# Optimization experiments

Measured on AMD Instinct MI355X. Metric: run time of the kernel, lower is better.

Reference implementation:

```python
import jax, jax.numpy as jnp
import numpy as np
import math

B, S, D, H, L = 2, 1024, 512, 8, 6
DK = D // H
DFF, V, MAXSEQ = 2048, 32000, 1024
EPS = 1e-6

def make_pe(max_len, d):
    pos = np.arange(max_len)[:, None].astype(np.float32)
    div = np.exp(np.arange(0, d, 2).astype(np.float32) * -(math.log(10000.0) / d))
    pe = np.zeros((max_len, d), np.float32)
    pe[:, 0::2] = np.sin(pos * div)
    pe[:, 1::2] = np.cos(pos * div)
    return jnp.asarray(pe)

PE = make_pe(5000, D)  # fixed sinusoidal buffer (non-learned)

def layer_norm(x, a, b):
    mean = jnp.mean(x, axis=-1, keepdims=True)
    std = jnp.std(x, axis=-1, ddof=1, keepdims=True)  # torch .std is unbiased
    return a * (x - mean) / (std + EPS) + b

def linear(x, W, b):
    # torch nn.Linear: y = x @ W.T + b, W is [out, in]
    return jnp.einsum('...i,oi->...o', x, W) + b

def rel_attention(q, k, v, mask4, pos_embeds):
    # q,k,v: [B,H,S,DK]; mask4: [B,1,S,S] int; pos_embeds: [H, MAXSEQ+1, DK]
    scale = 1.0 / math.sqrt(DK)
    scores = jnp.einsum('bhqd,bhkd->bhqk', q, k) * scale
    nz = (mask4 != 0).astype(jnp.int32)
    csum = (jnp.cumsum(mask4, axis=-1) - 1) * nz * S          # [B,1,S,S]
    offset = jnp.arange(S)[None, :]                            # [1,S] -> broadcasts over rows
    indices = (offset + csum) * nz                             # flat idx m*S + l into per-(b,h) [S,S]
    pe = pos_embeds[:, :S]                                     # [H,S,DK]
    rel = jnp.einsum('bhld,hmd->bhml', q, pe) * scale          # [B,H,S,S]
    idx = jnp.broadcast_to(indices, (B, H, S, S)).reshape(B, H, S * S)
    rel_g = jnp.take_along_axis(rel.reshape(B, H, S * S), idx, axis=-1)
    rel_g = rel_g.reshape(B, H, S, S) * nz.astype(scores.dtype)
    scores = jnp.where(mask4 == 0, -1e9, scores + rel_g)
    p = jax.nn.softmax(scores, axis=-1)
    return jnp.einsum('bhqk,bhkd->bhqd', p, v)

def reference(inp, inp_mask, emb, Wq, bq, Wk, bk, Wv, bv, Wo, bo, rel,
              ln1a, ln1b, ln2a, ln2b, W1, b1, W2, b2, lnfa, lnfb, Wg, bg):
    x = emb[inp] * math.sqrt(D) + PE[None, :S]   # embed + sinusoidal PE
    mask4 = inp_mask[:, None]                     # [B,1,S,S]
    for i in range(L):
        h = layer_norm(x, ln1a[i], ln1b[i])
        q = linear(h, Wq[i], bq[i]).reshape(B, S, H, DK).transpose(0, 2, 1, 3)
        k = linear(h, Wk[i], bk[i]).reshape(B, S, H, DK).transpose(0, 2, 1, 3)
        v = linear(h, Wv[i], bv[i]).reshape(B, S, H, DK).transpose(0, 2, 1, 3)
        a = rel_attention(q, k, v, mask4, rel[i])
        a = a.transpose(0, 2, 1, 3).reshape(B, S, D)
        x = x + linear(a, Wo[i], bo[i])
        h2 = layer_norm(x, ln2a[i], ln2b[i])
        x = x + linear(jax.nn.relu(linear(h2, W1[i], b1[i])), W2[i], b2[i])
    x = layer_norm(x, lnfa, lnfb)
    return jax.nn.log_softmax(linear(x, Wg, bg), axis=-1)

def setup_inputs() -> dict:
    key = jax.random.key(0)
    ks = jax.random.split(key, 16)
    rn = lambda k, shp, s=0.02: jax.random.normal(k, shp, jnp.float32) * s
    inp = jax.random.randint(ks[0], (B, S), 0, V, dtype=jnp.int32)
    inp_mask = jnp.broadcast_to(jnp.tril(jnp.ones((S, S), jnp.int32)), (B, S, S))
    return {
        'inp': inp, 'inp_mask': inp_mask,
        'emb': rn(ks[1], (V, D), 1.0),
        'Wq': rn(ks[2], (L, D, D)), 'bq': jnp.zeros((L, D), jnp.float32),
        'Wk': rn(ks[3], (L, D, D)), 'bk': jnp.zeros((L, D), jnp.float32),
        'Wv': rn(ks[4], (L, D, D)), 'bv': jnp.zeros((L, D), jnp.float32),
        'Wo': rn(ks[5], (L, D, D)), 'bo': jnp.zeros((L, D), jnp.float32),
        'rel': rn(ks[6], (L, H, MAXSEQ + 1, DK), 1.0),
        'ln1a': jnp.ones((L, D), jnp.float32), 'ln1b': jnp.zeros((L, D), jnp.float32),
        'ln2a': jnp.ones((L, D), jnp.float32), 'ln2b': jnp.zeros((L, D), jnp.float32),
        'W1': rn(ks[7], (L, DFF, D)), 'b1': jnp.zeros((L, DFF), jnp.float32),
        'W2': rn(ks[8], (L, D, DFF)), 'b2': jnp.zeros((L, D), jnp.float32),
        'lnfa': jnp.ones((D,), jnp.float32), 'lnfb': jnp.zeros((D,), jnp.float32),
        'Wg': rn(ks[9], (V, D)), 'bg': jnp.zeros((V,), jnp.float32),
    }
```

## Files before the change

kernel.cpp:

```cpp
#include <hip/hip_runtime.h>
#include <math.h>

typedef __bf16 bf16;
typedef __bf16 bf16x8 __attribute__((ext_vector_type(8)));
typedef __bf16 bf16x4 __attribute__((ext_vector_type(4)));
typedef __bf16 bf16x2 __attribute__((ext_vector_type(2)));
typedef float f32x4 __attribute__((ext_vector_type(4)));

#define B_ 2
#define S_ 1024
#define D_ 512
#define H_ 8
#define L_ 6
#define DK_ 64
#define DFF_ 2048
#define V_ 32000
#define MAXSEQ_ 1024
#define M_ 2048
#define QKV_ 1536

#define GLDS16(g, l) __builtin_amdgcn_global_load_lds((const __attribute__((address_space(1))) void*)(g), (__attribute__((address_space(3))) void*)(l), 16, 0, 0)

__device__ inline float blockReduceSum(float v, float* red) {
  for (int off = 32; off; off >>= 1) v += __shfl_xor(v, off, 64);
  int wid = threadIdx.x >> 6;
  __syncthreads();
  if ((threadIdx.x & 63) == 0) red[wid] = v;
  __syncthreads();
  return red[0] + red[1] + red[2] + red[3];
}

__global__ __launch_bounds__(256) void convw_kernel(const float* __restrict__ src,
                                                    bf16* __restrict__ dst, int n) {
  int i = (blockIdx.x * 256 + threadIdx.x) * 4;
  if (i < n) {
    float4 v = *(const float4*)(src + i);
    dst[i]     = (bf16)v.x;
    dst[i + 1] = (bf16)v.y;
    dst[i + 2] = (bf16)v.z;
    dst[i + 3] = (bf16)v.w;
  }
}

__global__ __launch_bounds__(256) void convqkv_kernel(const float* __restrict__ Wq,
                                                      const float* __restrict__ Wk,
                                                      const float* __restrict__ Wv,
                                                      bf16* __restrict__ dst) {
  int i = (blockIdx.x * 256 + threadIdx.x) * 4;
  int l = i / (QKV_ * D_);
  int rem = i - l * (QKV_ * D_);
  int r = rem >> 9;
  int c = i & (D_ - 1);
  int which = r >> 9, rr = r & 511;
  const float* src = (which == 0 ? Wq : which == 1 ? Wk : Wv) + ((size_t)l * D_ + rr) * D_ + c;
  float4 v = *(const float4*)src;
  dst[i]     = (bf16)v.x;
  dst[i + 1] = (bf16)v.y;
  dst[i + 2] = (bf16)v.z;
  dst[i + 3] = (bf16)v.w;
}

__global__ __launch_bounds__(256) void convbqkv_kernel(const float* __restrict__ bq,
                                                       const float* __restrict__ bk,
                                                       const float* __restrict__ bv,
                                                       float* __restrict__ dst) {
  int i = blockIdx.x * 256 + threadIdx.x;
  if (i >= L_ * QKV_) return;
  int l = i / QKV_, r = i - l * QKV_;
  int which = r >> 9, rr = r & 511;
  const float* s = (which == 0 ? bq : which == 1 ? bk : bv);
  dst[i] = s[l * D_ + rr];
}

__global__ __launch_bounds__(256) void embed_kernel(const int* __restrict__ inp,
                                                    const float* __restrict__ emb,
                                                    float* __restrict__ x) {
  int i = blockIdx.x * 256 + threadIdx.x;
  int d = i & (D_ - 1);
  int s = (i >> 9) & (S_ - 1);
  int b = i >> 19;
  int tok = inp[b * S_ + s];
  int j2 = d & ~1;
  float div = expf(-(float)j2 * (9.210340371976184f / (float)D_));
  float ang = (float)s * div;
  float pe = (d & 1) ? cosf(ang) : sinf(ang);
  x[i] = emb[(size_t)tok * D_ + d] * 22.627416997969522f + pe;
}

__global__ __launch_bounds__(256) void ln_kernel(const float* __restrict__ X,
                                                 const float* __restrict__ ga,
                                                 const float* __restrict__ gb,
                                                 bf16* __restrict__ out) {
  __shared__ float red[4];
  int row = blockIdx.x;
  const float* xr = X + (size_t)row * D_;
  int t = threadIdx.x;
  float x0 = xr[t], x1 = xr[t + 256];
  float mean = blockReduceSum(x0 + x1, red) * (1.0f / (float)D_);
  float d0 = x0 - mean, d1 = x1 - mean;
  float var = blockReduceSum(d0 * d0 + d1 * d1, red) * (1.0f / (float)(D_ - 1));
  float rs = 1.0f / (sqrtf(var) + 1e-6f);
  bf16* orow = out + (size_t)row * D_;
  orow[t]       = (bf16)(ga[t] * d0 * rs + gb[t]);
  orow[t + 256] = (bf16)(ga[t + 256] * d1 * rs + gb[t + 256]);
}

template <int EPI>
__global__ __launch_bounds__(256) void gemm128(const bf16* __restrict__ A,
                                               const bf16* __restrict__ W,
                                               const float* __restrict__ bias,
                                               void* __restrict__ Yv,
                                               const float* __restrict__ res,
                                               int M, int N, int K) {
  __shared__ __align__(16) bf16 As[128 * 32];
  __shared__ __align__(16) bf16 Bs[128 * 32];
  int t = threadIdx.x;
  int lane = t & 63, w = t >> 6;
  int n0 = blockIdx.x * 128, m0 = blockIdx.y * 128;
  int sr = lane >> 2, sc = (lane & 3) * 8;
  const bf16* ag0 = A + (size_t)(m0 + w * 16 + sr) * K + sc;
  const bf16* ag1 = A + (size_t)(m0 + (w + 4) * 16 + sr) * K + sc;
  const bf16* wg0 = W + (size_t)(n0 + w * 16 + sr) * K + sc;
  const bf16* wg1 = W + (size_t)(n0 + (w + 4) * 16 + sr) * K + sc;
  bf16* la0 = &As[w * 512];
  bf16* la1 = &As[(w + 4) * 512];
  bf16* lb0 = &Bs[w * 512];
  bf16* lb1 = &Bs[(w + 4) * 512];
  int wm = (w >> 1) * 64, wn = (w & 1) * 64;
  int fr = lane & 15, fk = (lane >> 4) * 8;
  f32x4 acc[4][4] = {};
  for (int kt = 0; kt < K; kt += 32) {
    GLDS16(ag0 + kt, la0);
    GLDS16(ag1 + kt, la1);
    GLDS16(wg0 + kt, lb0);
    GLDS16(wg1 + kt, lb1);
    __syncthreads();
    bf16x8 af[4], bfr[4];
    #pragma unroll
    for (int i = 0; i < 4; i++) af[i]  = *(const bf16x8*)&As[(wm + i * 16 + fr) * 32 + fk];
    #pragma unroll
    for (int i = 0; i < 4; i++) bfr[i] = *(const bf16x8*)&Bs[(wn + i * 16 + fr) * 32 + fk];
    #pragma unroll
    for (int mi = 0; mi < 4; mi++)
      #pragma unroll
      for (int ni = 0; ni < 4; ni++)
        acc[mi][ni] = __builtin_amdgcn_mfma_f32_16x16x32_bf16(af[mi], bfr[ni], acc[mi][ni], 0, 0, 0);
    __syncthreads();
  }
  int oc = lane & 15, orr = (lane >> 4) * 4;
  #pragma unroll
  for (int mi = 0; mi < 4; mi++)
    #pragma unroll
    for (int ni = 0; ni < 4; ni++)
      #pragma unroll
      for (int j = 0; j < 4; j++) {
        int row = m0 + wm + mi * 16 + orr + j;
        int col = n0 + wn + ni * 16 + oc;
        float val = acc[mi][ni][j] + bias[col];
        size_t idx = (size_t)row * N + col;
        if constexpr (EPI == 0)      ((float*)Yv)[idx] = val;
        else if constexpr (EPI == 1) ((bf16*)Yv)[idx] = (bf16)fmaxf(val, 0.0f);
        else if constexpr (EPI == 2) ((bf16*)Yv)[idx] = (bf16)val;
        else                         ((float*)Yv)[idx] = val + res[idx];
      }
}

__global__ __launch_bounds__(256) void relbias_kernel(const bf16* __restrict__ QKV,
                                                      const float* __restrict__ rel_l,
                                                      float* __restrict__ rb) {
  int i = blockIdx.x * 256 + threadIdx.x;
  int k = i & (S_ - 1);
  int h = (i >> 10) & (H_ - 1);
  int b = i >> 13;
  const bf16*  qp = QKV + ((size_t)(b * S_ + k)) * QKV_ + h * DK_;
  const float* rp = rel_l + ((size_t)h * (MAXSEQ_ + 1) + k) * DK_;
  float s = 0.f;
  #pragma unroll
  for (int j = 0; j < DK_; j++) s += (float)qp[j] * rp[j];
  rb[i] = s * 0.125f;
}

__device__ inline int swzb(int b) { return b ^ (((b >> 7) & 7) << 4); }

__global__ __launch_bounds__(128) void attn_kernel(const bf16* __restrict__ QKV,
                                                   const float* __restrict__ rb,
                                                   bf16* __restrict__ Aout) {
  __shared__ __align__(16) bf16 vt[64 * 64];
  __shared__ __align__(16) bf16 pts[2][16 * 64];
  __shared__ float rb_s[64];
  int t = threadIdx.x;
  int lane = t & 63, w = t >> 6;
  int ql = lane & 15, g = lane >> 4;
  int qb = blockIdx.x * 32;
  int h = blockIdx.y, b = blockIdx.z;
  const bf16* Qb = QKV + (size_t)(b * S_) * QKV_ + h * DK_;
  const bf16* Kb = Qb + D_;
  const bf16* Vb = Qb + 2 * D_;
  const float* rbb = rb + (b * H_ + h) * S_;
  int qg = qb + w * 16 + ql;

  bf16x8 qf0 = *(const bf16x8*)(Qb + (size_t)qg * QKV_ + 8 * g);
  bf16x8 qf1 = *(const bf16x8*)(Qb + (size_t)qg * QKV_ + 32 + 8 * g);

  char* vtb = (char*)vt;
  char* ptb = (char*)&pts[w][0];

  float mrun = -1e30f, lrun = 0.f;
  f32x4 acc[4] = {};

  int nkt = qb / 64 + 1;
  for (int kt = 0; kt < nkt; kt++) {
    int kb = kt * 64;
    bool last = (kt == nkt - 1);
    __syncthreads();
    #pragma unroll
    for (int i = 0; i < 2; i++) {
      int slot = t + 128 * i;
      int kp = slot >> 3, dc = slot & 7;
      bf16x8 r0 = *(const bf16x8*)(Vb + (size_t)(kb + 2 * kp) * QKV_ + dc * 8);
      bf16x8 r1 = *(const bf16x8*)(Vb + (size_t)(kb + 2 * kp + 1) * QKV_ + dc * 8);
      #pragma unroll
      for (int u = 0; u < 8; u++) {
        int d = dc * 8 + u;
        *(bf16x2*)(vtb + swzb(d * 128 + kp * 4)) = (bf16x2){r0[u], r1[u]};
      }
    }
    if (t < 64) rb_s[t] = rbb[kb + t];
    __syncthreads();

    f32x4 sc[4];
    #pragma unroll
    for (int ni = 0; ni < 4; ni++) {
      const bf16* krow = Kb + (size_t)(kb + 16 * ni + ql) * QKV_ + 8 * g;
      bf16x8 kf0 = *(const bf16x8*)(krow);
      bf16x8 kf1 = *(const bf16x8*)(krow + 32);
      f32x4 z = {};
      z = __builtin_amdgcn_mfma_f32_16x16x32_bf16(kf0, qf0, z, 0, 0, 0);
      z = __builtin_amdgcn_mfma_f32_16x16x32_bf16(kf1, qf1, z, 0, 0, 0);
      sc[ni] = z;
    }
    float tmax = -1e30f;
    #pragma unroll
    for (int ni = 0; ni < 4; ni++)
      #pragma unroll
      for (int j = 0; j < 4; j++) {
        int kloc = 16 * ni + 4 * g + j;
        float s = fmaf(sc[ni][j], 0.125f, rb_s[kloc]);
        if (last && (kb + kloc > qg)) s = -1e9f;
        sc[ni][j] = s;
        tmax = fmaxf(tmax, s);
      }
    tmax = fmaxf(tmax, __shfl_xor(tmax, 16, 64));
    tmax = fmaxf(tmax, __shfl_xor(tmax, 32, 64));
    float mnew = fmaxf(mrun, tmax);
    float fac = __expf(mrun - mnew);
    #pragma unroll
    for (int nd = 0; nd < 4; nd++)
      #pragma unroll
      for (int j = 0; j < 4; j++) acc[nd][j] *= fac;
    float tsum = 0.f;
    #pragma unroll
    for (int ni = 0; ni < 4; ni++)
      #pragma unroll
      for (int j = 0; j < 4; j++) {
        float p = __expf(sc[ni][j] - mnew);
        sc[ni][j] = p;
        tsum += p;
      }
    tsum += __shfl_xor(tsum, 16, 64);
    tsum += __shfl_xor(tsum, 32, 64);
    lrun = lrun * fac + tsum;
    mrun = mnew;

    #pragma unroll
    for (int ni = 0; ni < 4; ni++) {
      int byte0 = ql * 128 + 32 * ni + 8 * g;
      *(bf16x2*)(ptb + swzb(byte0))     = (bf16x2){(bf16)sc[ni][0], (bf16)sc[ni][1]};
      *(bf16x2*)(ptb + swzb(byte0 + 4)) = (bf16x2){(bf16)sc[ni][2], (bf16)sc[ni][3]};
    }
    bf16x8 pf0 = *(const bf16x8*)(ptb + swzb(ql * 128 + 16 * g));
    bf16x8 pf1 = *(const bf16x8*)(ptb + swzb(ql * 128 + 64 + 16 * g));
    #pragma unroll
    for (int nd = 0; nd < 4; nd++) {
      bf16x8 vf0 = *(const bf16x8*)(vtb + swzb((16 * nd + ql) * 128 + 16 * g));
      bf16x8 vf1 = *(const bf16x8*)(vtb + swzb((16 * nd + ql) * 128 + 64 + 16 * g));
      acc[nd] = __builtin_amdgcn_mfma_f32_16x16x32_bf16(vf0, pf0, acc[nd], 0, 0, 0);
      acc[nd] = __builtin_amdgcn_mfma_f32_16x16x32_bf16(vf1, pf1, acc[nd], 0, 0, 0);
    }
  }

  float inv = 1.0f / lrun;
  bf16* orow = Aout + (size_t)(b * S_ + qg) * D_ + h * DK_;
  #pragma unroll
  for (int nd = 0; nd < 4; nd++) {
    bf16x4 ov;
    #pragma unroll
    for (int j = 0; j < 4; j++) ov[j] = (bf16)(acc[nd][j] * inv);
    *(bf16x4*)(orow + 16 * nd + 4 * g) = ov;
  }
}

__global__ __launch_bounds__(256) void lsm_kernel(float* __restrict__ X) {
  __shared__ float redm[4], reds[4], sh[1];
  int row = blockIdx.x;
  float4* xr = (float4*)(X + (size_t)row * V_);
  int t = threadIdx.x;
  float m = -1e30f, s = 0.f;
  for (int i = t; i < V_ / 4; i += 256) {
    float4 v = xr[i];
    float m4 = fmaxf(fmaxf(v.x, v.y), fmaxf(v.z, v.w));
    if (m4 > m) { s *= __expf(m - m4); m = m4; }
    s += __expf(v.x - m) + __expf(v.y - m) + __expf(v.z - m) + __expf(v.w - m);
  }
  for (int off = 32; off; off >>= 1) {
    float m2 = __shfl_xor(m, off, 64);
    float s2 = __shfl_xor(s, off, 64);
    float mn = fmaxf(m, m2);
    s = s * __expf(m - mn) + s2 * __expf(m2 - mn);
    m = mn;
  }
  int wid = t >> 6;
  if ((t & 63) == 0) { redm[wid] = m; reds[wid] = s; }
  __syncthreads();
  if (t == 0) {
    float M2 = redm[0], SS = reds[0];
    for (int i2 = 1; i2 < 4; i2++) {
      float mn = fmaxf(M2, redm[i2]);
      SS = SS * __expf(M2 - mn) + reds[i2] * __expf(redm[i2] - mn);
      M2 = mn;
    }
    sh[0] = M2 + logf(SS);
  }
  __syncthreads();
  float lz = sh[0];
  for (int i = t; i < V_ / 4; i += 256) {
    float4 v = xr[i];
    v.x -= lz; v.y -= lz; v.z -= lz; v.w -= lz;
    xr[i] = v;
  }
}

extern "C" void kernel_launch(void* const* d_in, const int* in_sizes, int n_in,
                              void* d_out, int out_size, void* d_ws, size_t ws_size,
                              hipStream_t stream) {
  const int*   inp  = (const int*)d_in[0];
  const float* emb  = (const float*)d_in[2];
  const float* Wq   = (const float*)d_in[3];
  const float* bq   = (const float*)d_in[4];
  const float* Wk   = (const float*)d_in[5];
  const float* bk   = (const float*)d_in[6];
  const float* Wv   = (const float*)d_in[7];
  const float* bv   = (const float*)d_in[8];
  const float* Wo   = (const float*)d_in[9];
  const float* bo   = (const float*)d_in[10];
  const float* rel  = (const float*)d_in[11];
  const float* ln1a = (const float*)d_in[12];
  const float* ln1b = (const float*)d_in[13];
  const float* ln2a = (const float*)d_in[14];
  const float* ln2b = (const float*)d_in[15];
  const float* W1   = (const float*)d_in[16];
  const float* b1   = (const float*)d_in[17];
  const float* W2   = (const float*)d_in[18];
  const float* b2   = (const float*)d_in[19];
  const float* lnfa = (const float*)d_in[20];
  const float* lnfb = (const float*)d_in[21];
  const float* Wg   = (const float*)d_in[22];
  const float* bg   = (const float*)d_in[23];

  char* wp = (char*)d_ws;
  auto alloc = [&](size_t bytes) { void* p = wp; wp += (bytes + 255) & ~255ULL; return p; };
  float* x     = (float*)alloc((size_t)M_ * D_ * 4);
  bf16*  hbuf  = (bf16*) alloc((size_t)M_ * D_ * 2);
  bf16*  qkv   = (bf16*) alloc((size_t)M_ * QKV_ * 2);
  bf16*  abuf  = (bf16*) alloc((size_t)M_ * D_ * 2);
  bf16*  ffn   = (bf16*) alloc((size_t)M_ * DFF_ * 2);
  float* rbias = (float*)alloc((size_t)B_ * H_ * S_ * 4);
  bf16*  wqkvB = (bf16*) alloc((size_t)L_ * QKV_ * D_ * 2);
  float* bqkvB = (float*)alloc((size_t)L_ * QKV_ * 4);
  bf16*  woB   = (bf16*) alloc((size_t)L_ * D_ * D_ * 2);
  bf16*  w1B   = (bf16*) alloc((size_t)L_ * DFF_ * D_ * 2);
  bf16*  w2B   = (bf16*) alloc((size_t)L_ * D_ * DFF_ * 2);
  bf16*  wgB   = (bf16*) alloc((size_t)V_ * D_ * 2);

  convqkv_kernel<<<dim3(L_ * QKV_ * D_ / 1024), 256, 0, stream>>>(Wq, Wk, Wv, wqkvB);
  convbqkv_kernel<<<dim3((L_ * QKV_ + 255) / 256), 256, 0, stream>>>(bq, bk, bv, bqkvB);
  convw_kernel<<<dim3(L_ * D_ * D_ / 1024), 256, 0, stream>>>(Wo, woB, L_ * D_ * D_);
  convw_kernel<<<dim3(L_ * DFF_ * D_ / 1024), 256, 0, stream>>>(W1, w1B, L_ * DFF_ * D_);
  convw_kernel<<<dim3(L_ * D_ * DFF_ / 1024), 256, 0, stream>>>(W2, w2B, L_ * D_ * DFF_);
  convw_kernel<<<dim3(V_ * D_ / 1024), 256, 0, stream>>>(Wg, wgB, V_ * D_);

  embed_kernel<<<dim3((M_ * D_) / 256), 256, 0, stream>>>(inp, emb, x);

  dim3 gqkv(QKV_ / 128, M_ / 128);
  dim3 g512(D_ / 128, M_ / 128);
  dim3 gff(DFF_ / 128, M_ / 128);
  for (int l = 0; l < L_; l++) {
    ln_kernel<<<M_, 256, 0, stream>>>(x, ln1a + l * D_, ln1b + l * D_, hbuf);
    gemm128<2><<<gqkv, 256, 0, stream>>>(hbuf, wqkvB + (size_t)l * QKV_ * D_, bqkvB + l * QKV_, qkv, nullptr, M_, QKV_, D_);
    relbias_kernel<<<dim3((B_ * H_ * S_) / 256), 256, 0, stream>>>(qkv, rel + (size_t)l * H_ * (MAXSEQ_ + 1) * DK_, rbias);
    attn_kernel<<<dim3(S_ / 32, H_, B_), 128, 0, stream>>>(qkv, rbias, abuf);
    gemm128<3><<<g512, 256, 0, stream>>>(abuf, woB + (size_t)l * D_ * D_, bo + l * D_, x, x, M_, D_, D_);
    ln_kernel<<<M_, 256, 0, stream>>>(x, ln2a + l * D_, ln2b + l * D_, hbuf);
    gemm128<1><<<gff, 256, 0, stream>>>(hbuf, w1B + (size_t)l * DFF_ * D_, b1 + l * DFF_, ffn, nullptr, M_, DFF_, D_);
    gemm128<3><<<g512, 256, 0, stream>>>(ffn, w2B + (size_t)l * D_ * DFF_, b2 + l * D_, x, x, M_, D_, DFF_);
  }
  ln_kernel<<<M_, 256, 0, stream>>>(x, lnfa, lnfb, hbuf);
  dim3 gv(V_ / 128, M_ / 128);
  gemm128<0><<<gv, 256, 0, stream>>>(hbuf, wgB, bg, (float*)d_out, nullptr, M_, V_, D_);
  lsm_kernel<<<M_, 256, 0, stream>>>((float*)d_out);
}
```

Before: 1.606 ms.

## Rework GEMMs: double-buffered swizzled tiles, split-K atomics, bf16 logits for log-softmax

Replaces the 128x128 GEMM with a templated version that double-buffers shared-memory tiles and uses an XOR swizzle to avoid LDS bank conflicts. The QKV and FFN1 projections move to 64x128 tiles for more blocks. The residual GEMMs use 64x64 tiles with split-K and atomic accumulation into x. The vocabulary GEMM now writes bf16 logits to a scratch buffer that the log-softmax kernel reads and expands to fp32, halving the logit traffic. The costs are atomic contention, nondeterministic summation order, and lower logit precision before log-softmax.

After: 1.375 ms. 1.17x faster.

```diff
diff --git a/kernel.cpp b/kernel.cpp
--- a/kernel.cpp
+++ b/kernel.cpp
@@ -105,63 +105,84 @@
   orow[t + 256] = (bf16)(ga[t + 256] * d1 * rs + gb[t + 256]);
 }
 
-template <int EPI>
-__global__ __launch_bounds__(256) void gemm128(const bf16* __restrict__ A,
-                                               const bf16* __restrict__ W,
-                                               const float* __restrict__ bias,
-                                               void* __restrict__ Yv,
-                                               const float* __restrict__ res,
-                                               int M, int N, int K) {
-  __shared__ __align__(16) bf16 As[128 * 32];
-  __shared__ __align__(16) bf16 Bs[128 * 32];
-  int t = threadIdx.x;
-  int lane = t & 63, w = t >> 6;
-  int n0 = blockIdx.x * 128, m0 = blockIdx.y * 128;
-  int sr = lane >> 2, sc = (lane & 3) * 8;
-  const bf16* ag0 = A + (size_t)(m0 + w * 16 + sr) * K + sc;
-  const bf16* ag1 = A + (size_t)(m0 + (w + 4) * 16 + sr) * K + sc;
-  const bf16* wg0 = W + (size_t)(n0 + w * 16 + sr) * K + sc;
-  const bf16* wg1 = W + (size_t)(n0 + (w + 4) * 16 + sr) * K + sc;
-  bf16* la0 = &As[w * 512];
-  bf16* la1 = &As[(w + 4) * 512];
-  bf16* lb0 = &Bs[w * 512];
-  bf16* lb1 = &Bs[(w + 4) * 512];
-  int wm = (w >> 1) * 64, wn = (w & 1) * 64;
-  int fr = lane & 15, fk = (lane >> 4) * 8;
-  f32x4 acc[4][4] = {};
-  for (int kt = 0; kt < K; kt += 32) {
-    GLDS16(ag0 + kt, la0);
-    GLDS16(ag1 + kt, la1);
-    GLDS16(wg0 + kt, lb0);
-    GLDS16(wg1 + kt, lb1);
+template <int BM, int BN, int EPI, int SK>
+__global__ __launch_bounds__(256) void gemm_t(const bf16* __restrict__ A,
+                                              const bf16* __restrict__ W,
+                                              const float* __restrict__ bias,
+                                              void* __restrict__ Yv,
+                                              int M, int N, int K) {
+  constexpr int SMH = (BM + BN) * 32;
+  constexpr int NL  = (BM + BN) / 64;
+  constexpr int AF  = BM / 32, BF = BN / 32;
+  __shared__ __align__(16) bf16 sm[2 * SMH];
+  int t = threadIdx.x, lane = t & 63, w = t >> 6;
+  int n0 = blockIdx.x * BN, m0 = blockIdx.y * BM;
+  int koff = blockIdx.z * (K / SK);
+  int NT = (K / SK) / 32;
+  int wm = (w >> 1) * (BM / 2), wn = (w & 1) * (BN / 2);
+  int fr = lane & 15, g = lane >> 4;
+  int sr = lane >> 2;
+  int scq = ((lane & 3) ^ ((lane >> 2) & 3)) << 3;
+
+  f32x4 acc[AF][BF] = {};
+
+  auto stage = [&](int kt, int buf) {
+    bf16* base = sm + buf * SMH;
+    #pragma unroll
+    for (int i = 0; i < NL; i++) {
+      int chunk = i * 4 + w;
+      int kk = koff + kt * 32 + scq;
+      const bf16* gp;
+      if (i * 64 < BM) gp = A + (size_t)(m0 + chunk * 16 + sr) * K + kk;
+      else             gp = W + (size_t)(n0 + chunk * 16 - BM + sr) * K + kk;
+      GLDS16(gp, base + chunk * 512);
+    }
+  };
+
+  stage(0, 0);
+  int cur = 0;
+  for (int kt = 0; kt < NT; kt++) {
     __syncthreads();
-    bf16x8 af[4], bfr[4];
-    #pragma unroll
-    for (int i = 0; i < 4; i++) af[i]  = *(const bf16x8*)&As[(wm + i * 16 + fr) * 32 + fk];
-    #pragma unroll
-    for (int i = 0; i < 4; i++) bfr[i] = *(const bf16x8*)&Bs[(wn + i * 16 + fr) * 32 + fk];
-    #pragma unroll
-    for (int mi = 0; mi < 4; mi++)
-      #pragma unroll
-      for (int ni = 0; ni < 4; ni++)
-        acc[mi][ni] = __builtin_amdgcn_mfma_f32_16x16x32_bf16(af[mi], bfr[ni], acc[mi][ni], 0, 0, 0);
-    __syncthreads();
-  }
-  int oc = lane & 15, orr = (lane >> 4) * 4;
+    if (kt + 1 < NT) stage(kt + 1, cur ^ 1);
+    const bf16* As = sm + cur * SMH;
+    const bf16* Bs = As + BM * 32;
+    bf16x8 af[AF], bfv[BF];
+    #pragma unroll
+    for (int i = 0; i < AF; i++) {
+      int row = wm + i * 16 + fr;
+      af[i] = *(const bf16x8*)((const char*)As + row * 64 + ((g ^ (row & 3)) << 4));
+    }
+    #pragma unroll
+    for (int i = 0; i < BF; i++) {
+      int row = wn + i * 16 + fr;
+      bfv[i] = *(const bf16x8*)((const char*)Bs + row * 64 + ((g ^ (row & 3)) << 4));
+    }
+    #pragma unroll
+    for (int mi = 0; mi < AF; mi++)
+      #pragma unroll
+      for (int ni = 0; ni < BF; ni++)
+        acc[mi][ni] = __builtin_amdgcn_mfma_f32_16x16x32_bf16(af[mi], bfv[ni], acc[mi][ni], 0, 0, 0);
+    cur ^= 1;
+  }
+
+  int oc = lane & 15, orr = g * 4;
+  bool addb = (SK == 1) || (blockIdx.z == 0);
   #pragma unroll
-  for (int mi = 0; mi < 4; mi++)
-    #pragma unroll
-    for (int ni = 0; ni < 4; ni++)
+  for (int mi = 0; mi < AF; mi++)
+    #pragma unroll
+    for (int ni = 0; ni < BF; ni++)
       #pragma unroll
       for (int j = 0; j < 4; j++) {
         int row = m0 + wm + mi * 16 + orr + j;
         int col = n0 + wn + ni * 16 + oc;
-        float val = acc[mi][ni][j] + bias[col];
+        float val = acc[mi][ni][j];
         size_t idx = (size_t)row * N + col;
-        if constexpr (EPI == 0)      ((float*)Yv)[idx] = val;
-        else if constexpr (EPI == 1) ((bf16*)Yv)[idx] = (bf16)fmaxf(val, 0.0f);
-        else if constexpr (EPI == 2) ((bf16*)Yv)[idx] = (bf16)val;
-        else                         ((float*)Yv)[idx] = val + res[idx];
+        if constexpr (EPI == 1)      ((bf16*)Yv)[idx] = (bf16)fmaxf(val + bias[col], 0.0f);
+        else if constexpr (EPI == 2) ((bf16*)Yv)[idx] = (bf16)(val + bias[col]);
+        else {
+          if (addb) val += bias[col];
+          unsafeAtomicAdd((float*)Yv + idx, val);
+        }
       }
 }
 
@@ -300,17 +321,24 @@
   }
 }
 
-__global__ __launch_bounds__(256) void lsm_kernel(float* __restrict__ X) {
+__global__ __launch_bounds__(256) void lsm_kernel(const bf16* __restrict__ Lg,
+                                                  float* __restrict__ out) {
   __shared__ float redm[4], reds[4], sh[1];
   int row = blockIdx.x;
-  float4* xr = (float4*)(X + (size_t)row * V_);
+  const bf16x8* lr = (const bf16x8*)(Lg + (size_t)row * V_);
   int t = threadIdx.x;
   float m = -1e30f, s = 0.f;
-  for (int i = t; i < V_ / 4; i += 256) {
-    float4 v = xr[i];
-    float m4 = fmaxf(fmaxf(v.x, v.y), fmaxf(v.z, v.w));
-    if (m4 > m) { s *= __expf(m - m4); m = m4; }
-    s += __expf(v.x - m) + __expf(v.y - m) + __expf(v.z - m) + __expf(v.w - m);
+  for (int i = t; i < V_ / 8; i += 256) {
+    bf16x8 v = lr[i];
+    float f[8];
+    #pragma unroll
+    for (int e = 0; e < 8; e++) f[e] = (float)v[e];
+    float m8 = f[0];
+    #pragma unroll
+    for (int e = 1; e < 8; e++) m8 = fmaxf(m8, f[e]);
+    if (m8 > m) { s *= __expf(m - m8); m = m8; }
+    #pragma unroll
+    for (int e = 0; e < 8; e++) s += __expf(f[e] - m);
   }
   for (int off = 32; off; off >>= 1) {
     float m2 = __shfl_xor(m, off, 64);
@@ -333,10 +361,14 @@
   }
   __syncthreads();
   float lz = sh[0];
-  for (int i = t; i < V_ / 4; i += 256) {
-    float4 v = xr[i];
-    v.x -= lz; v.y -= lz; v.z -= lz; v.w -= lz;
-    xr[i] = v;
+  float4* orow = (float4*)(out + (size_t)row * V_);
+  for (int i = t; i < V_ / 8; i += 256) {
+    bf16x8 v = lr[i];
+    float4 a, b2;
+    a.x = (float)v[0] - lz; a.y = (float)v[1] - lz; a.z = (float)v[2] - lz; a.w = (float)v[3] - lz;
+    b2.x = (float)v[4] - lz; b2.y = (float)v[5] - lz; b2.z = (float)v[6] - lz; b2.w = (float)v[7] - lz;
+    orow[i * 2]     = a;
+    orow[i * 2 + 1] = b2;
   }
 }
 
@@ -375,6 +407,7 @@
   bf16*  abuf  = (bf16*) alloc((size_t)M_ * D_ * 2);
   bf16*  ffn   = (bf16*) alloc((size_t)M_ * DFF_ * 2);
   float* rbias = (float*)alloc((size_t)B_ * H_ * S_ * 4);
+  bf16*  lgbuf = (bf16*) alloc((size_t)M_ * V_ * 2);
   bf16*  wqkvB = (bf16*) alloc((size_t)L_ * QKV_ * D_ * 2);
   float* bqkvB = (float*)alloc((size_t)L_ * QKV_ * 4);
   bf16*  woB   = (bf16*) alloc((size_t)L_ * D_ * D_ * 2);
@@ -391,21 +424,22 @@
 
   embed_kernel<<<dim3((M_ * D_) / 256), 256, 0, stream>>>(inp, emb, x);
 
-  dim3 gqkv(QKV_ / 128, M_ / 128);
-  dim3 g512(D_ / 128, M_ / 128);
-  dim3 gff(DFF_ / 128, M_ / 128);
   for (int l = 0; l < L_; l++) {
     ln_kernel<<<M_, 256, 0, stream>>>(x, ln1a + l * D_, ln1b + l * D_, hbuf);
-    gemm128<2><<<gqkv, 256, 0, stream>>>(hbuf, wqkvB + (size_t)l * QKV_ * D_, bqkvB + l * QKV_, qkv, nullptr, M_, QKV_, D_);
+    gemm_t<64, 128, 2, 1><<<dim3(QKV_ / 128, M_ / 64), 256, 0, stream>>>(
+        hbuf, wqkvB + (size_t)l * QKV_ * D_, bqkvB + l * QKV_, qkv, M_, QKV_, D_);
     relbias_kernel<<<dim3((B_ * H_ * S_) / 256), 256, 0, stream>>>(qkv, rel + (size_t)l * H_ * (MAXSEQ_ + 1) * DK_, rbias);
     attn_kernel<<<dim3(S_ / 32, H_, B_), 128, 0, stream>>>(qkv, rbias, abuf);
-    gemm128<3><<<g512, 256, 0, stream>>>(abuf, woB + (size_t)l * D_ * D_, bo + l * D_, x, x, M_, D_, D_);
+    gemm_t<64, 64, 4, 2><<<dim3(D_ / 64, M_ / 64, 2), 256, 0, stream>>>(
+        abuf, woB + (size_t)l * D_ * D_, bo + l * D_, x, M_, D_, D_);
     ln_kernel<<<M_, 256, 0, stream>>>(x, ln2a + l * D_, ln2b + l * D_, hbuf);
-    gemm128<1><<<gff, 256, 0, stream>>>(hbuf, w1B + (size_t)l * DFF_ * D_, b1 + l * DFF_, ffn, nullptr, M_, DFF_, D_);
-    gemm128<3><<<g512, 256, 0, stream>>>(ffn, w2B + (size_t)l * D_ * DFF_, b2 + l * D_, x, x, M_, D_, DFF_);
+    gemm_t<64, 128, 1, 1><<<dim3(DFF_ / 128, M_ / 64), 256, 0, stream>>>(
+        hbuf, w1B + (size_t)l * DFF_ * D_, b1 + l * DFF_, ffn, M_, DFF_, D_);
+    gemm_t<64, 64, 4, 4><<<dim3(D_ / 64, M_ / 64, 4), 256, 0, stream>>>(
+        ffn, w2B + (size_t)l * D_ * DFF_, b2 + l * D_, x, M_, D_, DFF_);
   }
   ln_kernel<<<M_, 256, 0, stream>>>(x, lnfa, lnfb, hbuf);
-  dim3 gv(V_ / 128, M_ / 128);
-  gemm128<0><<<gv, 256, 0, stream>>>(hbuf, wgB, bg, (float*)d_out, nullptr, M_, V_, D_);
-  lsm_kernel<<<M_, 256, 0, stream>>>((float*)d_out);
-}
+  gemm_t<128, 128, 2, 1><<<dim3(V_ / 128, M_ / 128), 256, 0, stream>>>(
+      hbuf, wgB, bg, lgbuf, M_, V_, D_);
+  lsm_kernel<<<M_, 256, 0, stream>>>(lgbuf, (float*)d_out);
+}
```
